# Kernel optimization log

Hardware: AMD Instinct MI355X
Metric: run time of the kernel (lower is better)

The kernel has to match this reference:

```python
import jax, jax.numpy as jnp
import numpy as np

# Tap offsets (dy, dx) within the 3x3 footprint for each kernel_type.
# kernel_type 0 -> 5-tap skeleton (center + 4-neighbors), 1 -> full 3x3, else -> 3-tap row.
TAPS = {
    0: [(1, 1), (0, 1), (1, 0), (1, 2), (2, 1)],
    1: [(i, j) for i in range(3) for j in range(3)],
    2: [(1, 0), (1, 1), (1, 2)],
}

KERNEL_TYPE = 0
STRIDE = 1
PAD = 1
DIL = 1
SPATIAL = False


def setup_inputs() -> dict:
    key = jax.random.key(0)
    k1, k2 = jax.random.split(key)
    N, Ci, H, W = 16, 256, 64, 64
    Co, K = 256, len(TAPS[KERNEL_TYPE])
    x = jax.random.normal(k1, (N, Ci, H, W), dtype=jnp.float32)
    # kaiming-uniform-ish scale
    bound = np.sqrt(6.0 / (Ci * K))
    weight = jax.random.uniform(k2, (Co, Ci, K), dtype=jnp.float32, minval=-bound, maxval=bound)
    return {"x": x, "weight": weight, "step": 0}


def _spatial_conv(x, weight):
    # x: [N, Ci, H, W], weight: [Co, Ci, K]
    taps = TAPS[KERNEL_TYPE]
    N, Ci, H, W = x.shape
    Hout = (H + 2 * PAD - (DIL * 2 + 1)) // STRIDE + 1
    Wout = (W + 2 * PAD - (DIL * 2 + 1)) // STRIDE + 1
    xp = jnp.pad(x, ((0, 0), (0, 0), (PAD, PAD), (PAD, PAD)))
    outs = []
    for k, (dy, dx) in enumerate(taps):
        y0, x0 = dy * DIL, dx * DIL
        xs = xp[:, :, y0:y0 + (Hout - 1) * STRIDE + 1:STRIDE,
                      x0:x0 + (Wout - 1) * STRIDE + 1:STRIDE]  # [N, Ci, Hout, Wout]
        outs.append(jnp.einsum('nchw,oc->nohw', xs, weight[:, :, k]))
    return jnp.stack(outs, axis=0)  # [K, N, Co, Hout, Wout]


def reference(x, weight, step):
    out = _spatial_conv(x, weight)  # [K, N, Co, H, W]
    if SPATIAL:
        K, N, Co, Ho, Wo = out.shape
        out = jnp.transpose(out, (1, 0, 2, 3, 4)).reshape(N, K * Co, Ho, Wo)
    else:
        out = out.sum(axis=0)  # sum over taps -> [N, Co, H, W]
    return out
```

## Files before the change

kernel.cpp:

```cpp
#include <hip/hip_runtime.h>
#include <hip/hip_bf16.h>
#include <cstddef>

#define N_  16
#define CI  256
#define CO  256
#define KT  5

typedef __attribute__((ext_vector_type(8)))  short  short8;
typedef __attribute__((ext_vector_type(8)))  unsigned short ushort8;
typedef __attribute__((ext_vector_type(4)))  unsigned int uint4v;
typedef __attribute__((ext_vector_type(16))) float  floatx16;

static __device__ __forceinline__ unsigned short f2bf(float f) {
    union { float f; unsigned u; } v; v.f = f;
    unsigned r = v.u + 0x7fff + ((v.u >> 16) & 1);
    return (unsigned short)(r >> 16);
}

__global__ void wtrans_kernel(const float* __restrict__ w, unsigned short* __restrict__ wb) {
    int idx = blockIdx.x * 256 + threadIdx.x;
    if (idx >= KT * CO * CI) return;
    int k = idx >> 16;
    int rem = idx & 65535;
    int o = rem >> 8;
    int c = rem & 255;
    wb[idx] = f2bf(w[(size_t)o * (CI * KT) + c * KT + k]);
}

__global__ __launch_bounds__(256, 2) void conv_mfma(const float* __restrict__ x,
                                                    const unsigned short* __restrict__ wb,
                                                    float* __restrict__ out) {
    __shared__ ushort8 lds[2 * 1536 + 1];

    const int tid   = threadIdx.x;
    const int bx    = blockIdx.x;
    const int ohalf = bx & 1;
    const int hq    = (bx >> 1) & 15;
    const int n     = bx >> 5;
    const int h0    = hq * 4;
    const int lane  = tid & 63;
    const int wv    = tid >> 6;
    const int l31   = lane & 31;
    const int lh    = lane >> 5;
    const int owave   = ohalf * 128 + (wv & 1) * 64;
    const int rowbase = (wv >> 1) * 2;

    const int sw  = tid & 63;
    const int scg = (tid >> 6) & 3;

    if (tid == 0) lds[2 * 1536] = (ushort8)0;

    const float* xn = x + (size_t)n * CI * 4096;

    float xr[6][8];
    auto load_chunk = [&](int c) {
        #pragma unroll
        for (int i = 0; i < 6; ++i) {
            int hh = h0 + i - 1;
            if ((unsigned)hh < 64u) {
                const float* p = xn + (size_t)(c * 32 + scg * 8) * 4096 + hh * 64 + sw;
                #pragma unroll
                for (int e = 0; e < 8; ++e) xr[i][e] = p[(size_t)e * 4096];
            } else {
                #pragma unroll
                for (int e = 0; e < 8; ++e) xr[i][e] = 0.f;
            }
        }
    };
    auto write_chunk = [&](int b) {
        #pragma unroll
        for (int i = 0; i < 6; ++i) {
            uint4v v;
            #pragma unroll
            for (int e = 0; e < 4; ++e) {
                __hip_bfloat162 pk = __float22bfloat162_rn(
                    make_float2(xr[i][2 * e], xr[i][2 * e + 1]));
                union { __hip_bfloat162 h; unsigned u; } cv; cv.h = pk;
                v[e] = cv.u;
            }
            *(uint4v*)&lds[b * 1536 + i * 256 + scg * 64 + sw] = v;
        }
    };

    floatx16 acc[2][4];
    #pragma unroll
    for (int ot = 0; ot < 2; ++ot)
        #pragma unroll
        for (int t = 0; t < 4; ++t)
            #pragma unroll
            for (int e = 0; e < 16; ++e) acc[ot][t][e] = 0.f;

    const int laneoff = lh * 1024 + l31 * 16;
    const char* zcell = (const char*)&lds[2 * 1536];

    load_chunk(0);
    write_chunk(0);
    __syncthreads();

    for (int c = 0; c < 8; ++c) {
        const int cb = c & 1;
        if (c < 7) load_chunk(c + 1);

        const unsigned short* wbase = wb + (size_t)(owave + l31) * 256 + c * 32;
        const char* bufb = (const char*)&lds[cb * 1536];

        #pragma unroll
        for (int ks = 0; ks < 2; ++ks) {
            short8 a[2][KT];
            #pragma unroll
            for (int k = 0; k < KT; ++k)
                #pragma unroll
                for (int ot = 0; ot < 2; ++ot)
                    a[ot][k] = *(const short8*)(wbase + (size_t)k * 65536 + ot * 8192 + ks * 16 + lh * 8);

            #pragma unroll
            for (int k = 0; k < KT; ++k) {
                const int dy = (k == 1) ? 0 : (k == 4) ? 2 : 1;
                const int dx = (k == 2) ? 0 : (k == 3) ? 2 : 1;
                #pragma unroll
                for (int t = 0; t < 4; ++t) {
                    const int hr = t >> 1, wh = t & 1;
                    const int r  = rowbase + hr + dy;
                    const int wl = wh * 32 + l31 + dx - 1;
                    const char* bp = ((unsigned)wl < 64u)
                        ? bufb + (r * 4096 + ks * 2048 + (wh * 32 + dx - 1) * 16) + laneoff
                        : zcell;
                    const short8 bfrag = *(const short8*)bp;
                    acc[0][t] = __builtin_amdgcn_mfma_f32_32x32x16_bf16(a[0][k], bfrag, acc[0][t], 0, 0, 0);
                    acc[1][t] = __builtin_amdgcn_mfma_f32_32x32x16_bf16(a[1][k], bfrag, acc[1][t], 0, 0, 0);
                }
            }
        }

        if (c < 7) write_chunk(cb ^ 1);
        __syncthreads();
    }

    #pragma unroll
    for (int ot = 0; ot < 2; ++ot) {
        #pragma unroll
        for (int t = 0; t < 4; ++t) {
            const int hr = t >> 1, wh = t & 1;
            const int h = h0 + rowbase + hr;
            #pragma unroll
            for (int reg = 0; reg < 16; ++reg) {
                int o = owave + ot * 32 + (reg & 3) + 8 * (reg >> 2) + 4 * lh;
                out[(((size_t)n * CO + o) * 64 + h) * 64 + wh * 32 + l31] = acc[ot][t][reg];
            }
        }
    }
}

extern "C" void kernel_launch(void* const* d_in, const int* in_sizes, int n_in,
                              void* d_out, int out_size, void* d_ws, size_t ws_size,
                              hipStream_t stream) {
    const float* x = (const float*)d_in[0];
    const float* w = (const float*)d_in[1];
    float* out = (float*)d_out;

    unsigned short* wb = (unsigned short*)d_ws;

    wtrans_kernel<<<dim3((KT * CO * CI + 255) / 256), dim3(256), 0, stream>>>(w, wb);
    conv_mfma<<<dim3(N_ * 16 * 2), dim3(256), 0, stream>>>(x, wb, out);
}
```

Before: 159.2 us.

## Split x prefetch and weight loads into halves interleaved with MFMA tap groups

```diff
diff --git a/kernel.cpp b/kernel.cpp
--- a/kernel.cpp
+++ b/kernel.cpp
@@ -53,29 +53,29 @@
 
     const float* xn = x + (size_t)n * CI * 4096;
 
-    float xr[6][8];
-    auto load_chunk = [&](int c) {
+    float xh1[3][8], xh2[3][8];
+    auto load_half = [&](int c, int i0, float (&xr)[3][8]) {
         #pragma unroll
-        for (int i = 0; i < 6; ++i) {
-            int hh = h0 + i - 1;
-            if ((unsigned)hh < 64u) {
-                const float* p = xn + (size_t)(c * 32 + scg * 8) * 4096 + hh * 64 + sw;
-                #pragma unroll
-                for (int e = 0; e < 8; ++e) xr[i][e] = p[(size_t)e * 4096];
-            } else {
-                #pragma unroll
-                for (int e = 0; e < 8; ++e) xr[i][e] = 0.f;
-            }
+        for (int ii = 0; ii < 3; ++ii) {
+            int hh  = h0 + (i0 + ii) - 1;
+            int hcl = hh < 0 ? 0 : (hh > 63 ? 63 : hh);
+            const float* p = xn + (size_t)(c * 32 + scg * 8) * 4096 + hcl * 64 + sw;
+            #pragma unroll
+            for (int e = 0; e < 8; ++e) xr[ii][e] = p[(size_t)e * 4096];
         }
     };
-    auto write_chunk = [&](int b) {
+    auto write_half = [&](int b, int i0, float (&xr)[3][8]) {
         #pragma unroll
-        for (int i = 0; i < 6; ++i) {
+        for (int ii = 0; ii < 3; ++ii) {
+            int i  = i0 + ii;
+            int hh = h0 + i - 1;
+            const bool oob = (unsigned)hh >= 64u;
             uint4v v;
             #pragma unroll
             for (int e = 0; e < 4; ++e) {
-                __hip_bfloat162 pk = __float22bfloat162_rn(
-                    make_float2(xr[i][2 * e], xr[i][2 * e + 1]));
+                float f0 = oob ? 0.f : xr[ii][2 * e];
+                float f1 = oob ? 0.f : xr[ii][2 * e + 1];
+                __hip_bfloat162 pk = __float22bfloat162_rn(make_float2(f0, f1));
                 union { __hip_bfloat162 h; unsigned u; } cv; cv.h = pk;
                 v[e] = cv.u;
             }
@@ -94,30 +94,13 @@
     const int laneoff = lh * 1024 + l31 * 16;
     const char* zcell = (const char*)&lds[2 * 1536];
 
-    load_chunk(0);
-    write_chunk(0);
-    __syncthreads();
-
-    for (int c = 0; c < 8; ++c) {
-        const int cb = c & 1;
-        if (c < 7) load_chunk(c + 1);
-
-        const unsigned short* wbase = wb + (size_t)(owave + l31) * 256 + c * 32;
-        const char* bufb = (const char*)&lds[cb * 1536];
-
+    auto mfma_taps = [&](const char* bufb, const short8 a[][2][2], int klo, int khi) {
         #pragma unroll
-        for (int ks = 0; ks < 2; ++ks) {
-            short8 a[2][KT];
+        for (int k = klo; k < khi; ++k) {
+            const int dy = (k == 1) ? 0 : (k == 4) ? 2 : 1;
+            const int dx = (k == 2) ? 0 : (k == 3) ? 2 : 1;
             #pragma unroll
-            for (int k = 0; k < KT; ++k)
-                #pragma unroll
-                for (int ot = 0; ot < 2; ++ot)
-                    a[ot][k] = *(const short8*)(wbase + (size_t)k * 65536 + ot * 8192 + ks * 16 + lh * 8);
-
-            #pragma unroll
-            for (int k = 0; k < KT; ++k) {
-                const int dy = (k == 1) ? 0 : (k == 4) ? 2 : 1;
-                const int dx = (k == 2) ? 0 : (k == 3) ? 2 : 1;
+            for (int ks = 0; ks < 2; ++ks) {
                 #pragma unroll
                 for (int t = 0; t < 4; ++t) {
                     const int hr = t >> 1, wh = t & 1;
@@ -127,14 +110,57 @@
                         ? bufb + (r * 4096 + ks * 2048 + (wh * 32 + dx - 1) * 16) + laneoff
                         : zcell;
                     const short8 bfrag = *(const short8*)bp;
-                    acc[0][t] = __builtin_amdgcn_mfma_f32_32x32x16_bf16(a[0][k], bfrag, acc[0][t], 0, 0, 0);
-                    acc[1][t] = __builtin_amdgcn_mfma_f32_32x32x16_bf16(a[1][k], bfrag, acc[1][t], 0, 0, 0);
+                    acc[0][t] = __builtin_amdgcn_mfma_f32_32x32x16_bf16(a[k - klo][ks][0], bfrag, acc[0][t], 0, 0, 0);
+                    acc[1][t] = __builtin_amdgcn_mfma_f32_32x32x16_bf16(a[k - klo][ks][1], bfrag, acc[1][t], 0, 0, 0);
                 }
             }
         }
+    };
 
-        if (c < 7) write_chunk(cb ^ 1);
-        __syncthreads();
+    load_half(0, 0, xh1);
+    load_half(0, 3, xh2);
+    write_half(0, 0, xh1);
+    write_half(0, 3, xh2);
+    __syncthreads();
+
+    for (int c = 0; c < 8; ++c) {
+        const int cb = c & 1;
+        const bool pf = (c < 7);
+        const unsigned short* wbase = wb + (size_t)(owave + l31) * 256 + c * 32;
+        const char* bufb = (const char*)&lds[cb * 1536];
+
+        short8 a01[2][2][2];
+        #pragma unroll
+        for (int k = 0; k < 2; ++k)
+            #pragma unroll
+            for (int ks = 0; ks < 2; ++ks)
+                #pragma unroll
+                for (int ot = 0; ot < 2; ++ot)
+                    a01[k][ks][ot] = *(const short8*)(wbase + (size_t)k * 65536 + ot * 8192 + ks * 16 + lh * 8);
+
+        if (pf) load_half(c + 1, 0, xh1);
+
+        mfma_taps(bufb, a01, 0, 2);
+
+        short8 a234[3][2][2];
+        #pragma unroll
+        for (int k = 2; k < 5; ++k)
+            #pragma unroll
+            for (int ks = 0; ks < 2; ++ks)
+                #pragma unroll
+                for (int ot = 0; ot < 2; ++ot)
+                    a234[k - 2][ks][ot] = *(const short8*)(wbase + (size_t)k * 65536 + ot * 8192 + ks * 16 + lh * 8);
+
+        if (pf) load_half(c + 1, 3, xh2);
+
+        if (pf) write_half(cb ^ 1, 0, xh1);
+
+        mfma_taps(bufb, a234, 2, 5);
+
+        if (pf) {
+            write_half(cb ^ 1, 3, xh2);
+            __syncthreads();
+        }
     }
 
     #pragma unroll
```

Measured after the change: 160.2 us. No clear change (+0.6%).

## Pre-convert input to bf16 and stage via async global-to-LDS loads

Applied to the files above, without the earlier changes.

```diff
diff --git a/kernel.cpp b/kernel.cpp
--- a/kernel.cpp
+++ b/kernel.cpp
@@ -1,5 +1,4 @@
 #include <hip/hip_runtime.h>
-#include <hip/hip_bf16.h>
 #include <cstddef>
 
 #define N_  16
@@ -9,8 +8,10 @@
 
 typedef __attribute__((ext_vector_type(8)))  short  short8;
 typedef __attribute__((ext_vector_type(8)))  unsigned short ushort8;
-typedef __attribute__((ext_vector_type(4)))  unsigned int uint4v;
 typedef __attribute__((ext_vector_type(16))) float  floatx16;
+
+typedef const __attribute__((address_space(1))) unsigned int gas_uint;
+typedef __attribute__((address_space(3))) unsigned int las_uint;
 
 static __device__ __forceinline__ unsigned short f2bf(float f) {
     union { float f; unsigned u; } v; v.f = f;
@@ -28,125 +29,144 @@
     wb[idx] = f2bf(w[(size_t)o * (CI * KT) + c * KT + k]);
 }
 
-__global__ __launch_bounds__(256, 2) void conv_mfma(const float* __restrict__ x,
+__global__ __launch_bounds__(256) void xtrans_kernel(const float* __restrict__ x,
+                                                     unsigned short* __restrict__ xb) {
+    int idx = blockIdx.x * 256 + threadIdx.x;
+    int w  = idx & 63;
+    int h  = (idx >> 6) & 63;
+    int cg = (idx >> 12) & 31;
+    int n  = idx >> 17;
+    const float* xp = x + (((size_t)n * CI + cg * 8) * 64 + h) * 64 + w;
+    ushort8 v;
+    #pragma unroll
+    for (int e = 0; e < 8; ++e) v[e] = f2bf(xp[(size_t)e * 4096]);
+    *(ushort8*)(xb + (size_t)idx * 8) = v;
+}
+
+__global__ __launch_bounds__(256, 3) void conv_mfma(const unsigned short* __restrict__ xb,
                                                     const unsigned short* __restrict__ wb,
                                                     float* __restrict__ out) {
-    __shared__ ushort8 lds[2 * 1536 + 1];
+    __shared__ ushort8 lds[2 * 1024 + 1];
 
-    const int tid   = threadIdx.x;
-    const int bx    = blockIdx.x;
-    const int ohalf = bx & 1;
-    const int hq    = (bx >> 1) & 15;
-    const int n     = bx >> 5;
-    const int h0    = hq * 4;
-    const int lane  = tid & 63;
-    const int wv    = tid >> 6;
-    const int l31   = lane & 31;
-    const int lh    = lane >> 5;
-    const int owave   = ohalf * 128 + (wv & 1) * 64;
-    const int rowbase = (wv >> 1) * 2;
+    const int tid  = threadIdx.x;
+    const int bx   = blockIdx.x;
+    const int oh   = bx & 1;
+    const int hp   = (bx >> 1) & 31;
+    const int n    = bx >> 6;
+    const int h0   = hp * 2;
+    const int lane = tid & 63;
+    const int wv   = tid >> 6;
+    const int l31  = lane & 31;
+    const int lh   = lane >> 5;
+    const int osub = wv & 1;
+    const int row  = wv >> 1;
+    const int obase0 = oh * 128 + osub * 64;
 
-    const int sw  = tid & 63;
-    const int scg = (tid >> 6) & 3;
+    const int sw = tid & 63;
+    const int spart = tid >> 6;
 
-    if (tid == 0) lds[2 * 1536] = (ushort8)0;
+    if (tid == 0) lds[2048] = (ushort8)0;
+    if (hp == 0)  { lds[0 * 1024 + tid] = (ushort8)0; lds[1 * 1024 + tid] = (ushort8)0; }
+    if (hp == 31) { lds[0 * 1024 + 768 + tid] = (ushort8)0; lds[1 * 1024 + 768 + tid] = (ushort8)0; }
 
-    const float* xn = x + (size_t)n * CI * 4096;
-
-    float xr[6][8];
-    auto load_chunk = [&](int c) {
+    auto stage = [&](int c, int b) {
         #pragma unroll
-        for (int i = 0; i < 6; ++i) {
-            int hh = h0 + i - 1;
+        for (int r = 0; r < 4; ++r) {
+            const int hh = h0 + r - 1;
             if ((unsigned)hh < 64u) {
-                const float* p = xn + (size_t)(c * 32 + scg * 8) * 4096 + hh * 64 + sw;
-                #pragma unroll
-                for (int e = 0; e < 8; ++e) xr[i][e] = p[(size_t)e * 4096];
-            } else {
-                #pragma unroll
-                for (int e = 0; e < 8; ++e) xr[i][e] = 0.f;
+                const unsigned short* g =
+                    xb + (((size_t)(n * 32 + c * 4 + spart) * 64 + hh) * 64 + sw) * 8;
+                __builtin_amdgcn_global_load_lds(
+                    (gas_uint*)g,
+                    (las_uint*)&lds[b * 1024 + r * 256 + spart * 64 + sw],
+                    16, 0, 0);
             }
         }
     };
-    auto write_chunk = [&](int b) {
+
+    floatx16 acc[2][2];
+    #pragma unroll
+    for (int ot = 0; ot < 2; ++ot)
         #pragma unroll
-        for (int i = 0; i < 6; ++i) {
-            uint4v v;
+        for (int wt = 0; wt < 2; ++wt)
             #pragma unroll
-            for (int e = 0; e < 4; ++e) {
-                __hip_bfloat162 pk = __float22bfloat162_rn(
-                    make_float2(xr[i][2 * e], xr[i][2 * e + 1]));
-                union { __hip_bfloat162 h; unsigned u; } cv; cv.h = pk;
-                v[e] = cv.u;
+            for (int e = 0; e < 16; ++e) acc[ot][wt][e] = 0.f;
+
+    const char* zcell = (const char*)&lds[2048];
+    const int laneoff = l31 * 16;
+
+    auto mfma_tap = [&](const char* bufb, const short8 a[2][2], int k) {
+        const int dy = (k == 1) ? 0 : (k == 4) ? 2 : 1;
+        const int dx = (k == 2) ? 0 : (k == 3) ? 2 : 1;
+        const int r  = row + dy;
+        #pragma unroll
+        for (int ks = 0; ks < 2; ++ks) {
+            #pragma unroll
+            for (int wt = 0; wt < 2; ++wt) {
+                const int wlb = wt * 32 + dx - 1;
+                const int wl  = wlb + l31;
+                const char* bp = ((unsigned)wl < 64u)
+                    ? bufb + (r * 4096 + (ks * 2 + lh) * 1024 + wlb * 16) + laneoff
+                    : zcell;
+                const short8 bfrag = *(const short8*)bp;
+                acc[0][wt] = __builtin_amdgcn_mfma_f32_32x32x16_bf16(a[ks][0], bfrag, acc[0][wt], 0, 0, 0);
+                acc[1][wt] = __builtin_amdgcn_mfma_f32_32x32x16_bf16(a[ks][1], bfrag, acc[1][wt], 0, 0, 0);
             }
-            *(uint4v*)&lds[b * 1536 + i * 256 + scg * 64 + sw] = v;
         }
     };
 
-    floatx16 acc[2][4];
-    #pragma unroll
-    for (int ot = 0; ot < 2; ++ot)
-        #pragma unroll
-        for (int t = 0; t < 4; ++t)
-            #pragma unroll
-            for (int e = 0; e < 16; ++e) acc[ot][t][e] = 0.f;
-
-    const int laneoff = lh * 1024 + l31 * 16;
-    const char* zcell = (const char*)&lds[2 * 1536];
-
-    load_chunk(0);
-    write_chunk(0);
-    __syncthreads();
+    stage(0, 0);
 
     for (int c = 0; c < 8; ++c) {
         const int cb = c & 1;
-        if (c < 7) load_chunk(c + 1);
+        __syncthreads();
 
-        const unsigned short* wbase = wb + (size_t)(owave + l31) * 256 + c * 32;
-        const char* bufb = (const char*)&lds[cb * 1536];
+        const unsigned short* wbase = wb + (size_t)(obase0 + l31) * 256 + c * 32 + lh * 8;
 
+        short8 a01[2][2][2];
         #pragma unroll
-        for (int ks = 0; ks < 2; ++ks) {
-            short8 a[2][KT];
+        for (int k = 0; k < 2; ++k)
             #pragma unroll
-            for (int k = 0; k < KT; ++k)
+            for (int ks = 0; ks < 2; ++ks)
                 #pragma unroll
                 for (int ot = 0; ot < 2; ++ot)
-                    a[ot][k] = *(const short8*)(wbase + (size_t)k * 65536 + ot * 8192 + ks * 16 + lh * 8);
+                    a01[k][ks][ot] = *(const short8*)(wbase + (size_t)k * 65536 + ot * 8192 + ks * 16);
 
+        if (c < 7) stage(c + 1, cb ^ 1);
+
+        const char* bufb = (const char*)&lds[cb * 1024];
+        mfma_tap(bufb, a01[0], 0);
+        mfma_tap(bufb, a01[1], 1);
+
+        short8 a23[2][2][2];
+        #pragma unroll
+        for (int k = 2; k < 4; ++k)
             #pragma unroll
-            for (int k = 0; k < KT; ++k) {
-                const int dy = (k == 1) ? 0 : (k == 4) ? 2 : 1;
-                const int dx = (k == 2) ? 0 : (k == 3) ? 2 : 1;
+            for (int ks = 0; ks < 2; ++ks)
                 #pragma unroll
-                for (int t = 0; t < 4; ++t) {
-                    const int hr = t >> 1, wh = t & 1;
-                    const int r  = rowbase + hr + dy;
-                    const int wl = wh * 32 + l31 + dx - 1;
-                    const char* bp = ((unsigned)wl < 64u)
-                        ? bufb + (r * 4096 + ks * 2048 + (wh * 32 + dx - 1) * 16) + laneoff
-                        : zcell;
-                    const short8 bfrag = *(const short8*)bp;
-                    acc[0][t] = __builtin_amdgcn_mfma_f32_32x32x16_bf16(a[0][k], bfrag, acc[0][t], 0, 0, 0);
-                    acc[1][t] = __builtin_amdgcn_mfma_f32_32x32x16_bf16(a[1][k], bfrag, acc[1][t], 0, 0, 0);
-                }
-            }
-        }
+                for (int ot = 0; ot < 2; ++ot)
+                    a23[k - 2][ks][ot] = *(const short8*)(wbase + (size_t)k * 65536 + ot * 8192 + ks * 16);
+        mfma_tap(bufb, a23[0], 2);
+        mfma_tap(bufb, a23[1], 3);
 
-        if (c < 7) write_chunk(cb ^ 1);
-        __syncthreads();
+        short8 a4[2][2];
+        #pragma unroll
+        for (int ks = 0; ks < 2; ++ks)
+            #pragma unroll
+            for (int ot = 0; ot < 2; ++ot)
+                a4[ks][ot] = *(const short8*)(wbase + (size_t)4 * 65536 + ot * 8192 + ks * 16);
+        mfma_tap(bufb, a4, 4);
     }
 
+    const int h = h0 + row;
     #pragma unroll
     for (int ot = 0; ot < 2; ++ot) {
         #pragma unroll
-        for (int t = 0; t < 4; ++t) {
-            const int hr = t >> 1, wh = t & 1;
-            const int h = h0 + rowbase + hr;
+        for (int wt = 0; wt < 2; ++wt) {
             #pragma unroll
             for (int reg = 0; reg < 16; ++reg) {
-                int o = owave + ot * 32 + (reg & 3) + 8 * (reg >> 2) + 4 * lh;
-                out[(((size_t)n * CO + o) * 64 + h) * 64 + wh * 32 + l31] = acc[ot][t][reg];
+                int o = obase0 + ot * 32 + (reg & 3) + 8 * (reg >> 2) + 4 * lh;
+                out[(((size_t)n * CO + o) * 64 + h) * 64 + wt * 32 + l31] = acc[ot][wt][reg];
             }
         }
     }
@@ -160,7 +180,9 @@
     float* out = (float*)d_out;
 
     unsigned short* wb = (unsigned short*)d_ws;
+    unsigned short* xb = (unsigned short*)((char*)d_ws + (size_t)KT * CO * CI * 2);
 
     wtrans_kernel<<<dim3((KT * CO * CI + 255) / 256), dim3(256), 0, stream>>>(w, wb);
-    conv_mfma<<<dim3(N_ * 16 * 2), dim3(256), 0, stream>>>(x, wb, out);
+    xtrans_kernel<<<dim3(16 * 32 * 64 * 64 / 256), dim3(256), 0, stream>>>(x, xb);
+    conv_mfma<<<dim3(N_ * 32 * 2), dim3(256), 0, stream>>>(xb, wb, out);
 }
```

Measured after the change: 207.3 us. +30.2%, slower.
